# Kernel optimization log

Measured on AMD Instinct MI355X. Metric: run time of the kernel, lower is better.

The kernel has to match this reference:

```python
import jax, jax.numpy as jnp
import numpy as np

EPS = 1e-5

def _layernorm(x, g, b):
    mu = jnp.mean(x, axis=-1, keepdims=True)
    var = jnp.mean(jnp.square(x - mu), axis=-1, keepdims=True)
    return (x - mu) / jnp.sqrt(var + EPS) * g + b

def setup_inputs() -> dict:
    key = jax.random.key(0)
    ks = jax.random.split(key, 8)
    B, T, E, H, Dh, F = 4, 2048, 1024, 16, 64, 4096
    s = lambda fan: 1.0 / np.sqrt(fan)
    return {
        "x":  jax.random.normal(ks[0], (B, T, E), jnp.float32),
        "Wq": jax.random.normal(ks[1], (H, E, Dh), jnp.float32) * s(E),
        "Wk": jax.random.normal(ks[2], (H, E, Dh), jnp.float32) * s(E),
        "Wv": jax.random.normal(ks[3], (H, E, Dh), jnp.float32) * s(E),
        "Wo": jax.random.normal(ks[4], (E, E), jnp.float32) * s(E),
        "bo": jnp.zeros((E,), jnp.float32),
        "W1": jax.random.normal(ks[5], (E, F), jnp.float32) * s(E),
        "b1": jnp.zeros((F,), jnp.float32),
        "W2": jax.random.normal(ks[6], (F, E), jnp.float32) * s(F),
        "b2": jnp.zeros((E,), jnp.float32),
        "g1": jnp.ones((E,), jnp.float32),
        "bt1": jnp.zeros((E,), jnp.float32),
        "g2": jnp.ones((E,), jnp.float32),
        "bt2": jnp.zeros((E,), jnp.float32),
    }

def reference(x, Wq, Wk, Wv, Wo, bo, W1, b1, W2, b2, g1, bt1, g2, bt2):
    B, T, E = x.shape
    # --- pre-LN multi-head attention (dropout = identity in eval) ---
    h = _layernorm(x, g1, bt1)
    q = jnp.einsum('btc,hcd->bhtd', h, Wq)
    k = jnp.einsum('btc,hcd->bhtd', h, Wk)
    v = jnp.einsum('btc,hcd->bhtd', h, Wv)
    # NOTE: original scales by embed_size**-0.5 (input channel c), not head_size
    scores = jnp.einsum('bhtd,bhsd->bhts', q, k) * (E ** -0.5)
    causal = jnp.tril(jnp.ones((T, T), bool))
    scores = jnp.where(causal, scores, -jnp.inf)
    attn = jax.nn.softmax(scores, axis=-1)
    ctx = jnp.einsum('bhts,bhsd->bhtd', attn, v)
    ctx = ctx.transpose(0, 2, 1, 3).reshape(B, T, E)  # concat heads
    x = x + ctx @ Wo + bo
    # --- pre-LN feed-forward ---
    h2 = _layernorm(x, g2, bt2)
    x = x + jax.nn.relu(h2 @ W1 + b1) @ W2 + b2
    return x
```

## Files before the change

kernel.cpp:

```cpp
#include <hip/hip_runtime.h>

typedef unsigned short u16;
typedef __attribute__((ext_vector_type(8))) short bf16x8;
typedef __attribute__((ext_vector_type(4))) short bf16x4;
typedef __attribute__((ext_vector_type(4))) float f32x4;

#define LOG2E 1.4426950408889634f

__device__ __forceinline__ float b2f(u16 u) {
  union { unsigned int i; float f; } x; x.i = ((unsigned int)u) << 16; return x.f;
}
__device__ __forceinline__ u16 f2b(float f) {
  unsigned int i = __float_as_uint(f);
  unsigned int r = (i + 0x7FFFu + ((i >> 16) & 1u)) >> 16;
  return (u16)r;
}
__device__ __forceinline__ void stc(u16* C, size_t i, float v) { C[i] = f2b(v); }
__device__ __forceinline__ void stc(float* C, size_t i, float v) { C[i] = v; }

__device__ __forceinline__ bool is_f32(const unsigned* probe) {
  return probe[0] == 0x3F800000u;
}
__device__ __forceinline__ float ldin(const void* p, size_t i, bool f32) {
  return f32 ? ((const float*)p)[i] : b2f(((const u16*)p)[i]);
}

__device__ __forceinline__ void gld_lds16(const void* g, void* l) {
  __builtin_amdgcn_global_load_lds(
      (const __attribute__((address_space(1))) unsigned int*)g,
      (__attribute__((address_space(3))) unsigned int*)l, 16, 0, 0);
}

__device__ __forceinline__ void lds_wave_fence() {
  __asm__ volatile("s_waitcnt lgkmcnt(0)" ::: "memory");
}

__global__ __launch_bounds__(256) void ln_kernel(
    const void* __restrict__ x, int x_raw,
    const void* __restrict__ g, const void* __restrict__ b,
    u16* __restrict__ y, const unsigned* __restrict__ probe) {
  __shared__ float red[4];
  const bool f32 = is_f32(probe);
  int row = blockIdx.x, tid = threadIdx.x;
  int w = tid >> 6;
  float f0, f1, f2, f3;
  if (x_raw && f32) {
    const float* xr = (const float*)x + (size_t)row * 1024 + tid * 4;
    float4 v = *(const float4*)xr;
    f0 = v.x; f1 = v.y; f2 = v.z; f3 = v.w;
  } else {
    const u16* xr = (const u16*)x + (size_t)row * 1024 + tid * 4;
    bf16x4 v = *(const bf16x4*)xr;
    f0 = b2f((u16)v[0]); f1 = b2f((u16)v[1]); f2 = b2f((u16)v[2]); f3 = b2f((u16)v[3]);
  }
  float s = f0 + f1 + f2 + f3;
  #pragma unroll
  for (int o = 32; o >= 1; o >>= 1) s += __shfl_xor(s, o, 64);
  if ((tid & 63) == 0) red[w] = s;
  __syncthreads();
  float mean = (red[0] + red[1] + red[2] + red[3]) * (1.0f / 1024.0f);
  __syncthreads();
  float d0 = f0 - mean, d1 = f1 - mean, d2 = f2 - mean, d3 = f3 - mean;
  float vs = d0 * d0 + d1 * d1 + d2 * d2 + d3 * d3;
  #pragma unroll
  for (int o = 32; o >= 1; o >>= 1) vs += __shfl_xor(vs, o, 64);
  if ((tid & 63) == 0) red[w] = vs;
  __syncthreads();
  float var = (red[0] + red[1] + red[2] + red[3]) * (1.0f / 1024.0f);
  float rstd = rsqrtf(var + 1e-5f);
  int c = tid * 4;
  float o0 = d0 * rstd * ldin(g, c + 0, f32) + ldin(b, c + 0, f32);
  float o1 = d1 * rstd * ldin(g, c + 1, f32) + ldin(b, c + 1, f32);
  float o2 = d2 * rstd * ldin(g, c + 2, f32) + ldin(b, c + 2, f32);
  float o3 = d3 * rstd * ldin(g, c + 3, f32) + ldin(b, c + 3, f32);
  bf16x4 ov; ov[0] = (short)f2b(o0); ov[1] = (short)f2b(o1);
  ov[2] = (short)f2b(o2); ov[3] = (short)f2b(o3);
  *(bf16x4*)(y + (size_t)row * 1024 + c) = ov;
}

__global__ __launch_bounds__(256) void repack_t(
    const void* __restrict__ src, u16* __restrict__ dst, int N, int K,
    const unsigned* __restrict__ probe) {
  const bool f32 = is_f32(probe);
  int flat = blockIdx.x * 256 + threadIdx.x;
  int n = flat % N;
  int c0 = (flat / N) * 8;
  bf16x8 t;
  #pragma unroll
  for (int j = 0; j < 8; j++) t[j] = (short)f2b(ldin(src, (size_t)(c0 + j) * N + n, f32));
  *(bf16x8*)&dst[(size_t)n * K + c0] = t;
}

__global__ __launch_bounds__(256) void repack_qkv(
    const void* __restrict__ Wq, const void* __restrict__ Wk,
    const void* __restrict__ Wv, u16* __restrict__ dst,
    const unsigned* __restrict__ probe) {
  const bool f32 = is_f32(probe);
  int flat = blockIdx.x * 256 + threadIdx.x;
  int n = flat % 3072;
  int c0 = (flat / 3072) * 8;
  const void* W = (n < 1024) ? Wq : (n < 2048) ? Wk : Wv;
  int nn = n & 1023;
  int hn = nn >> 6, d = nn & 63;
  bf16x8 t;
  #pragma unroll
  for (int j = 0; j < 8; j++)
    t[j] = (short)f2b(ldin(W, (size_t)hn * 65536 + (size_t)(c0 + j) * 64 + d, f32));
  *(bf16x8*)&dst[(size_t)n * 1024 + c0] = t;
}

template <int EPI, typename CT>
__global__ __launch_bounds__(256) void gemm_bt(
    const u16* __restrict__ A, const u16* __restrict__ Bt, CT* __restrict__ C,
    int M, int N, int K, const void* __restrict__ bias,
    const void* __restrict__ res, int res_raw,
    const unsigned* __restrict__ probe) {
  __shared__ __align__(16) u16 sA[128 * 32];
  __shared__ __align__(16) u16 sB[128 * 32];
  const bool f32 = is_f32(probe);
  int tid = threadIdx.x;
  int w = tid >> 6, lane = tid & 63;
  int l15 = lane & 15, q4 = lane >> 4;
  int bm = blockIdx.x * 128, bn = blockIdx.y * 128;
  int wm = (w & 1) * 64, wn = (w >> 1) * 64;
  f32x4 acc[4][4] = {};
  for (int k0 = 0; k0 < K; k0 += 32) {
    #pragma unroll
    for (int j = 0; j < 2; ++j) {
      int c = j * 256 + tid;
      int row = c >> 2, ck = (c & 3) * 8;
      gld_lds16(A + (size_t)(bm + row) * K + k0 + ck, &sA[c * 8]);
    }
    #pragma unroll
    for (int j = 0; j < 2; ++j) {
      int c = j * 256 + tid;
      int row = c >> 2, ck = (c & 3) * 8;
      gld_lds16(Bt + (size_t)(bn + row) * K + k0 + ck, &sB[c * 8]);
    }
    __syncthreads();
    bf16x8 af[4], bf[4];
    #pragma unroll
    for (int i = 0; i < 4; i++) af[i] = *(const bf16x8*)&sA[(wm + i * 16 + l15) * 32 + q4 * 8];
    #pragma unroll
    for (int j = 0; j < 4; j++) bf[j] = *(const bf16x8*)&sB[(wn + j * 16 + l15) * 32 + q4 * 8];
    #pragma unroll
    for (int i = 0; i < 4; i++)
      #pragma unroll
      for (int j = 0; j < 4; j++)
        acc[i][j] = __builtin_amdgcn_mfma_f32_16x16x32_bf16(af[i], bf[j], acc[i][j], 0, 0, 0);
    __syncthreads();
  }
  #pragma unroll
  for (int i = 0; i < 4; i++) {
    int rg = bm + wm + i * 16 + q4 * 4;
    #pragma unroll
    for (int j = 0; j < 4; j++) {
      int cg = bn + wn + j * 16 + l15;
      float bv = (EPI > 0) ? ldin(bias, cg, f32) : 0.0f;
      #pragma unroll
      for (int r = 0; r < 4; r++) {
        float v = acc[i][j][r];
        if (EPI == 1) v += bv + ldin(res, (size_t)(rg + r) * N + cg, res_raw && f32);
        if (EPI == 2) { v += bv; v = fmaxf(v, 0.0f); }
        stc(C, (size_t)(rg + r) * N + cg, v);
      }
    }
  }
}

__global__ __launch_bounds__(256) void attn_kernel(
    const u16* __restrict__ qkv, u16* __restrict__ ctx, int T) {
  __shared__ __align__(16) u16 sK[64 * 64];
  __shared__ __align__(16) u16 sVt[64 * 64];
  __shared__ __align__(16) u16 sP[4 * 16 * 64];
  int tid = threadIdx.x;
  int w = tid >> 6, lane = tid & 63;
  int l15 = lane & 15, q4 = lane >> 4;
  int qtile = blockIdx.x, h = blockIdx.y, b = blockIdx.z;
  int bbase = b * T;
  int qt0 = qtile * 64;

  const u16* qrow = qkv + (size_t)(bbase + qt0 + w * 16 + l15) * 3072 + h * 64;
  bf16x8 qf0 = *(const bf16x8*)(qrow + q4 * 8);
  bf16x8 qf1 = *(const bf16x8*)(qrow + 32 + q4 * 8);

  f32x4 o[4] = {};
  float m4[4] = {-1e30f, -1e30f, -1e30f, -1e30f};
  float l4[4] = {0.f, 0.f, 0.f, 0.f};

  for (int kt = 0; kt <= qtile; ++kt) {
    __syncthreads();
    #pragma unroll
    for (int j = 0; j < 2; ++j) {
      int c = j * 256 + tid;
      int tr = c >> 3, dc = (c & 7) * 8;
      *(bf16x8*)&sK[tr * 64 + dc] =
          *(const bf16x8*)(qkv + (size_t)(bbase + kt * 64 + tr) * 3072 + 1024 + h * 64 + dc);
    }
    {
      int t = tid & 63, dbase = (tid >> 6) * 16;
      const u16* vsrc = qkv + (size_t)(bbase + kt * 64 + t) * 3072 + 2048 + h * 64 + dbase;
      bf16x8 v0 = *(const bf16x8*)vsrc;
      bf16x8 v1 = *(const bf16x8*)(vsrc + 8);
      #pragma unroll
      for (int jj = 0; jj < 8; jj++) {
        sVt[(dbase + jj) * 64 + t] = (u16)v0[jj];
        sVt[(dbase + 8 + jj) * 64 + t] = (u16)v1[jj];
      }
    }
    __syncthreads();

    f32x4 s[4];
    #pragma unroll
    for (int j = 0; j < 4; j++) {
      bf16x8 kf0 = *(const bf16x8*)&sK[(j * 16 + l15) * 64 + q4 * 8];
      bf16x8 kf1 = *(const bf16x8*)&sK[(j * 16 + l15) * 64 + 32 + q4 * 8];
      f32x4 z = {0.f, 0.f, 0.f, 0.f};
      z = __builtin_amdgcn_mfma_f32_16x16x32_bf16(qf0, kf0, z, 0, 0, 0);
      z = __builtin_amdgcn_mfma_f32_16x16x32_bf16(qf1, kf1, z, 0, 0, 0);
      s[j] = z;
    }
    float sv[4][4];
    #pragma unroll
    for (int j = 0; j < 4; j++)
      #pragma unroll
      for (int r = 0; r < 4; r++) {
        float v = s[j][r] * 0.03125f;
        if (kt == qtile && (j * 16 + l15) > (w * 16 + q4 * 4 + r)) v = -1e30f;
        sv[j][r] = v;
      }
    float tm4[4];
    #pragma unroll
    for (int r = 0; r < 4; r++)
      tm4[r] = fmaxf(fmaxf(sv[0][r], sv[1][r]), fmaxf(sv[2][r], sv[3][r]));
    #pragma unroll
    for (int off = 8; off >= 1; off >>= 1)
      #pragma unroll
      for (int r = 0; r < 4; r++) tm4[r] = fmaxf(tm4[r], __shfl_xor(tm4[r], off, 64));
    float al4[4];
    #pragma unroll
    for (int r = 0; r < 4; r++) {
      float mn = fmaxf(m4[r], tm4[r]);
      al4[r] = exp2f((m4[r] - mn) * LOG2E);
      m4[r] = mn;
    }
    float p[4][4], ts4[4];
    #pragma unroll
    for (int j = 0; j < 4; j++)
      #pragma unroll
      for (int r = 0; r < 4; r++) p[j][r] = exp2f((sv[j][r] - m4[r]) * LOG2E);
    #pragma unroll
    for (int r = 0; r < 4; r++) ts4[r] = p[0][r] + p[1][r] + p[2][r] + p[3][r];
    #pragma unroll
    for (int off = 8; off >= 1; off >>= 1)
      #pragma unroll
      for (int r = 0; r < 4; r++) ts4[r] += __shfl_xor(ts4[r], off, 64);
    #pragma unroll
    for (int r = 0; r < 4; r++) l4[r] = l4[r] * al4[r] + ts4[r];
    #pragma unroll
    for (int j = 0; j < 4; j++)
      #pragma unroll
      for (int r = 0; r < 4; r++) o[j][r] *= al4[r];
    #pragma unroll
    for (int j = 0; j < 4; j++)
      #pragma unroll
      for (int r = 0; r < 4; r++)
        sP[w * 1024 + (q4 * 4 + r) * 64 + j * 16 + l15] = f2b(p[j][r]);
    lds_wave_fence();
    bf16x8 pf0 = *(const bf16x8*)&sP[w * 1024 + l15 * 64 + q4 * 8];
    bf16x8 pf1 = *(const bf16x8*)&sP[w * 1024 + l15 * 64 + 32 + q4 * 8];
    #pragma unroll
    for (int j = 0; j < 4; j++) {
      bf16x8 vf0 = *(const bf16x8*)&sVt[(j * 16 + l15) * 64 + q4 * 8];
      bf16x8 vf1 = *(const bf16x8*)&sVt[(j * 16 + l15) * 64 + 32 + q4 * 8];
      o[j] = __builtin_amdgcn_mfma_f32_16x16x32_bf16(pf0, vf0, o[j], 0, 0, 0);
      o[j] = __builtin_amdgcn_mfma_f32_16x16x32_bf16(pf1, vf1, o[j], 0, 0, 0);
    }
  }
  #pragma unroll
  for (int j = 0; j < 4; j++)
    #pragma unroll
    for (int r = 0; r < 4; r++) {
      size_t addr = (size_t)(bbase + qt0 + w * 16 + q4 * 4 + r) * 1024 + h * 64 + j * 16 + l15;
      ctx[addr] = f2b(o[j][r] / l4[r]);
    }
}

extern "C" void kernel_launch(void* const* d_in, const int* in_sizes, int n_in,
                              void* d_out, int out_size, void* d_ws, size_t ws_size,
                              hipStream_t stream) {
  (void)in_sizes; (void)n_in; (void)out_size; (void)ws_size;
  const void* x   = d_in[0];
  const void* Wq  = d_in[1];
  const void* Wk  = d_in[2];
  const void* Wv  = d_in[3];
  const void* Wo  = d_in[4];
  const void* bo  = d_in[5];
  const void* W1  = d_in[6];
  const void* b1  = d_in[7];
  const void* W2  = d_in[8];
  const void* b2  = d_in[9];
  const void* g1  = d_in[10];
  const void* bt1 = d_in[11];
  const void* g2  = d_in[12];
  const void* bt2 = d_in[13];
  const unsigned* probe = (const unsigned*)g1;
  float* out = (float*)d_out;

  const int BT = 8192, T = 2048;
  char* ws = (char*)d_ws;
  u16* hln    = (u16*)(ws);
  u16* qkv    = (u16*)(ws + 16777216);
  u16* ctx    = (u16*)(ws + 16777216 + 50331648);
  u16* a      = (u16*)(ws + 16777216);
  u16* x1     = (u16*)(ws + 83886080);
  u16* wqkv_t = (u16*)(ws + 100663296);
  u16* wo_t   = (u16*)(ws + 106954752);
  u16* w1_t   = (u16*)(ws + 109051904);
  u16* w2_t   = (u16*)(ws + 117440512);

  repack_qkv<<<1536, 256, 0, stream>>>(Wq, Wk, Wv, wqkv_t, probe);
  repack_t<<<512, 256, 0, stream>>>(Wo, wo_t, 1024, 1024, probe);
  repack_t<<<2048, 256, 0, stream>>>(W1, w1_t, 4096, 1024, probe);
  repack_t<<<2048, 256, 0, stream>>>(W2, w2_t, 1024, 4096, probe);

  ln_kernel<<<BT, 256, 0, stream>>>(x, 1, g1, bt1, hln, probe);
  gemm_bt<0, u16><<<dim3(64, 24), 256, 0, stream>>>(hln, wqkv_t, qkv, BT, 3072, 1024,
                                                    nullptr, nullptr, 0, probe);
  attn_kernel<<<dim3(32, 16, 4), 256, 0, stream>>>(qkv, ctx, T);
  gemm_bt<1, u16><<<dim3(64, 8), 256, 0, stream>>>(ctx, wo_t, x1, BT, 1024, 1024,
                                                   bo, x, 1, probe);
  ln_kernel<<<BT, 256, 0, stream>>>(x1, 0, g2, bt2, hln, probe);
  gemm_bt<2, u16><<<dim3(64, 32), 256, 0, stream>>>(hln, w1_t, a, BT, 4096, 1024,
                                                    b1, nullptr, 0, probe);
  gemm_bt<1, float><<<dim3(64, 8), 256, 0, stream>>>(a, w2_t, out, BT, 1024, 4096,
                                                     b2, x1, 0, probe);
}
```

Measured before the change: 827.3 us.

## Restructure attention: 128-row query tiles, padded LDS, shuffle V transpose, balanced scheduling

The attention kernel now processes 128 query rows per block (two 16-row groups per wave), so each K/V tile loaded into LDS is reused by twice as many queries. LDS rows are padded to 68 elements to reduce bank conflicts, and V is transposed in registers via lane shuffles before a vectorized LDS store. Global loads are issued before the barrier to overlap with the previous iteration. The grid is flattened with a causal-balancing tile order. It also skips fully masked sub-tiles and uses the hardware exp2. In exchange, register pressure rises and there are half as many blocks.

```diff
diff --git a/kernel.cpp b/kernel.cpp
--- a/kernel.cpp
+++ b/kernel.cpp
@@ -33,6 +33,21 @@
 
 __device__ __forceinline__ void lds_wave_fence() {
   __asm__ volatile("s_waitcnt lgkmcnt(0)" ::: "memory");
+}
+
+__device__ __forceinline__ void tr8(unsigned a[4], int lane) {
+  unsigned p0, p1, p2, p3;
+  p0 = __shfl_xor((int)a[0], 1, 64); p1 = __shfl_xor((int)a[1], 1, 64);
+  p2 = __shfl_xor((int)a[2], 1, 64); p3 = __shfl_xor((int)a[3], 1, 64);
+  unsigned sel = (lane & 1) ? 0x3276u : 0x5410u;
+  a[0] = __byte_perm(a[0], p0, sel); a[1] = __byte_perm(a[1], p1, sel);
+  a[2] = __byte_perm(a[2], p2, sel); a[3] = __byte_perm(a[3], p3, sel);
+  p0 = __shfl_xor((int)a[0], 2, 64); p1 = __shfl_xor((int)a[1], 2, 64);
+  p2 = __shfl_xor((int)a[2], 2, 64); p3 = __shfl_xor((int)a[3], 2, 64);
+  if (lane & 2) { a[0] = p1; a[2] = p3; } else { a[1] = p0; a[3] = p2; }
+  p0 = __shfl_xor((int)a[0], 4, 64); p1 = __shfl_xor((int)a[1], 4, 64);
+  p2 = __shfl_xor((int)a[2], 4, 64); p3 = __shfl_xor((int)a[3], 4, 64);
+  if (lane & 4) { a[0] = p2; a[1] = p3; } else { a[2] = p0; a[3] = p1; }
 }
 
 __global__ __launch_bounds__(256) void ln_kernel(
@@ -170,120 +185,164 @@
 
 __global__ __launch_bounds__(256) void attn_kernel(
     const u16* __restrict__ qkv, u16* __restrict__ ctx, int T) {
-  __shared__ __align__(16) u16 sK[64 * 64];
-  __shared__ __align__(16) u16 sVt[64 * 64];
-  __shared__ __align__(16) u16 sP[4 * 16 * 64];
+  __shared__ __align__(16) u16 sK[64 * 68];
+  __shared__ __align__(16) u16 sVt[64 * 68];
+  __shared__ __align__(16) u16 sP[8 * 16 * 68];
   int tid = threadIdx.x;
   int w = tid >> 6, lane = tid & 63;
   int l15 = lane & 15, q4 = lane >> 4;
-  int qtile = blockIdx.x, h = blockIdx.y, b = blockIdx.z;
-  int bbase = b * T;
-  int qt0 = qtile * 64;
-
-  const u16* qrow = qkv + (size_t)(bbase + qt0 + w * 16 + l15) * 3072 + h * 64;
-  bf16x8 qf0 = *(const bf16x8*)(qrow + q4 * 8);
-  bf16x8 qf1 = *(const bf16x8*)(qrow + 32 + q4 * 8);
-
-  f32x4 o[4] = {};
-  float m4[4] = {-1e30f, -1e30f, -1e30f, -1e30f};
-  float l4[4] = {0.f, 0.f, 0.f, 0.f};
-
-  for (int kt = 0; kt <= qtile; ++kt) {
-    __syncthreads();
+
+  int n = blockIdx.x;
+  int qi = n & 15;
+  int h = (n >> 4) & 15;
+  int b = (n >> 8) & 3;
+  int qbase = (qi & 1) ? (qi >> 1) : (15 - (qi >> 1));
+  int qt = (qbase + 7 * b) & 15;
+  int qt0 = qt * 128;
+  int mb[2] = {qt0 + w * 16, qt0 + 64 + w * 16};
+  size_t b3072 = (size_t)(b * T) * 3072;
+
+  bf16x8 qf[2][2];
+  #pragma unroll
+  for (int m = 0; m < 2; m++) {
+    const u16* qr = qkv + b3072 + (size_t)(mb[m] + l15) * 3072 + h * 64;
+    qf[m][0] = *(const bf16x8*)(qr + q4 * 8);
+    qf[m][1] = *(const bf16x8*)(qr + 32 + q4 * 8);
+  }
+  f32x4 o[2][4] = {};
+  float mx[2][4], ls[2][4];
+  #pragma unroll
+  for (int m = 0; m < 2; m++)
+    #pragma unroll
+    for (int r = 0; r < 4; r++) { mx[m][r] = -1e30f; ls[m][r] = 0.f; }
+
+  int ktmax = 2 * qt + 1;
+  for (int kt = 0; kt <= ktmax; ++kt) {
+    int s0 = kt * 64;
+    bf16x8 kreg[2]; int krow[2], kcol[2];
     #pragma unroll
     for (int j = 0; j < 2; ++j) {
       int c = j * 256 + tid;
-      int tr = c >> 3, dc = (c & 7) * 8;
-      *(bf16x8*)&sK[tr * 64 + dc] =
-          *(const bf16x8*)(qkv + (size_t)(bbase + kt * 64 + tr) * 3072 + 1024 + h * 64 + dc);
-    }
+      krow[j] = c >> 3; kcol[j] = (c & 7) * 8;
+      kreg[j] = *(const bf16x8*)(qkv + b3072 + (size_t)(s0 + krow[j]) * 3072 + 1024 + h * 64 + kcol[j]);
+    }
+    unsigned va[4], vb[4];
     {
-      int t = tid & 63, dbase = (tid >> 6) * 16;
-      const u16* vsrc = qkv + (size_t)(bbase + kt * 64 + t) * 3072 + 2048 + h * 64 + dbase;
-      bf16x8 v0 = *(const bf16x8*)vsrc;
-      bf16x8 v1 = *(const bf16x8*)(vsrc + 8);
-      #pragma unroll
-      for (int jj = 0; jj < 8; jj++) {
-        sVt[(dbase + jj) * 64 + t] = (u16)v0[jj];
-        sVt[(dbase + 8 + jj) * 64 + t] = (u16)v1[jj];
-      }
+      const u16* vs = qkv + b3072 + (size_t)(s0 + lane) * 3072 + 2048 + h * 64 + w * 16;
+      *(bf16x8*)va = *(const bf16x8*)vs;
+      *(bf16x8*)vb = *(const bf16x8*)(vs + 8);
     }
     __syncthreads();
-
-    f32x4 s[4];
-    #pragma unroll
-    for (int j = 0; j < 4; j++) {
-      bf16x8 kf0 = *(const bf16x8*)&sK[(j * 16 + l15) * 64 + q4 * 8];
-      bf16x8 kf1 = *(const bf16x8*)&sK[(j * 16 + l15) * 64 + 32 + q4 * 8];
+    #pragma unroll
+    for (int j = 0; j < 2; ++j)
+      *(bf16x8*)&sK[krow[j] * 68 + kcol[j]] = kreg[j];
+    tr8(va, lane); tr8(vb, lane);
+    {
+      int dd = w * 16 + (lane & 7), t0 = (lane >> 3) * 8;
+      *(bf16x8*)&sVt[dd * 68 + t0] = *(bf16x8*)va;
+      *(bf16x8*)&sVt[(dd + 8) * 68 + t0] = *(bf16x8*)vb;
+    }
+    __syncthreads();
+
+    bool act0 = (s0 <= mb[0] + 15);
+    f32x4 s[2][4];
+    #pragma unroll
+    for (int j = 0; j < 4; ++j) {
+      bf16x8 k0 = *(const bf16x8*)&sK[(j * 16 + l15) * 68 + q4 * 8];
+      bf16x8 k1 = *(const bf16x8*)&sK[(j * 16 + l15) * 68 + 32 + q4 * 8];
+      if (act0) {
+        f32x4 z = {0.f, 0.f, 0.f, 0.f};
+        z = __builtin_amdgcn_mfma_f32_16x16x32_bf16(qf[0][0], k0, z, 0, 0, 0);
+        s[0][j] = __builtin_amdgcn_mfma_f32_16x16x32_bf16(qf[0][1], k1, z, 0, 0, 0);
+      }
       f32x4 z = {0.f, 0.f, 0.f, 0.f};
-      z = __builtin_amdgcn_mfma_f32_16x16x32_bf16(qf0, kf0, z, 0, 0, 0);
-      z = __builtin_amdgcn_mfma_f32_16x16x32_bf16(qf1, kf1, z, 0, 0, 0);
-      s[j] = z;
-    }
-    float sv[4][4];
-    #pragma unroll
-    for (int j = 0; j < 4; j++)
-      #pragma unroll
-      for (int r = 0; r < 4; r++) {
-        float v = s[j][r] * 0.03125f;
-        if (kt == qtile && (j * 16 + l15) > (w * 16 + q4 * 4 + r)) v = -1e30f;
-        sv[j][r] = v;
-      }
-    float tm4[4];
-    #pragma unroll
-    for (int r = 0; r < 4; r++)
-      tm4[r] = fmaxf(fmaxf(sv[0][r], sv[1][r]), fmaxf(sv[2][r], sv[3][r]));
-    #pragma unroll
-    for (int off = 8; off >= 1; off >>= 1)
-      #pragma unroll
-      for (int r = 0; r < 4; r++) tm4[r] = fmaxf(tm4[r], __shfl_xor(tm4[r], off, 64));
-    float al4[4];
-    #pragma unroll
-    for (int r = 0; r < 4; r++) {
-      float mn = fmaxf(m4[r], tm4[r]);
-      al4[r] = exp2f((m4[r] - mn) * LOG2E);
-      m4[r] = mn;
-    }
-    float p[4][4], ts4[4];
-    #pragma unroll
-    for (int j = 0; j < 4; j++)
-      #pragma unroll
-      for (int r = 0; r < 4; r++) p[j][r] = exp2f((sv[j][r] - m4[r]) * LOG2E);
-    #pragma unroll
-    for (int r = 0; r < 4; r++) ts4[r] = p[0][r] + p[1][r] + p[2][r] + p[3][r];
-    #pragma unroll
-    for (int off = 8; off >= 1; off >>= 1)
-      #pragma unroll
-      for (int r = 0; r < 4; r++) ts4[r] += __shfl_xor(ts4[r], off, 64);
-    #pragma unroll
-    for (int r = 0; r < 4; r++) l4[r] = l4[r] * al4[r] + ts4[r];
-    #pragma unroll
-    for (int j = 0; j < 4; j++)
-      #pragma unroll
-      for (int r = 0; r < 4; r++) o[j][r] *= al4[r];
-    #pragma unroll
-    for (int j = 0; j < 4; j++)
-      #pragma unroll
-      for (int r = 0; r < 4; r++)
-        sP[w * 1024 + (q4 * 4 + r) * 64 + j * 16 + l15] = f2b(p[j][r]);
+      z = __builtin_amdgcn_mfma_f32_16x16x32_bf16(qf[1][0], k0, z, 0, 0, 0);
+      s[1][j] = __builtin_amdgcn_mfma_f32_16x16x32_bf16(qf[1][1], k1, z, 0, 0, 0);
+    }
+    #pragma unroll
+    for (int m = 0; m < 2; ++m) {
+      if (m == 0 && !act0) continue;
+      int mbm = mb[m];
+      if (s0 + 63 > mbm) {
+        #pragma unroll
+        for (int j = 0; j < 4; ++j)
+          #pragma unroll
+          for (int r = 0; r < 4; ++r) {
+            float v = s[m][j][r] * 0.03125f;
+            if (s0 + j * 16 + l15 > mbm + q4 * 4 + r) v = -1e30f;
+            s[m][j][r] = v;
+          }
+      } else {
+        #pragma unroll
+        for (int j = 0; j < 4; ++j)
+          #pragma unroll
+          for (int r = 0; r < 4; ++r) s[m][j][r] *= 0.03125f;
+      }
+      float tm[4];
+      #pragma unroll
+      for (int r = 0; r < 4; ++r)
+        tm[r] = fmaxf(fmaxf(s[m][0][r], s[m][1][r]), fmaxf(s[m][2][r], s[m][3][r]));
+      #pragma unroll
+      for (int off = 8; off >= 1; off >>= 1)
+        #pragma unroll
+        for (int r = 0; r < 4; ++r) tm[r] = fmaxf(tm[r], __shfl_xor(tm[r], off, 64));
+      float al[4], ts[4];
+      #pragma unroll
+      for (int r = 0; r < 4; ++r) {
+        float mn = fmaxf(mx[m][r], tm[r]);
+        al[r] = __builtin_amdgcn_exp2f((mx[m][r] - mn) * LOG2E);
+        mx[m][r] = mn; ts[r] = 0.f;
+      }
+      int pbase = (w * 2 + m) * 1088;
+      #pragma unroll
+      for (int j = 0; j < 4; ++j)
+        #pragma unroll
+        for (int r = 0; r < 4; ++r) {
+          float p = __builtin_amdgcn_exp2f((s[m][j][r] - mx[m][r]) * LOG2E);
+          ts[r] += p;
+          sP[pbase + (q4 * 4 + r) * 68 + j * 16 + l15] = f2b(p);
+        }
+      #pragma unroll
+      for (int off = 8; off >= 1; off >>= 1)
+        #pragma unroll
+        for (int r = 0; r < 4; ++r) ts[r] += __shfl_xor(ts[r], off, 64);
+      #pragma unroll
+      for (int r = 0; r < 4; ++r) ls[m][r] = ls[m][r] * al[r] + ts[r];
+      #pragma unroll
+      for (int j = 0; j < 4; ++j)
+        #pragma unroll
+        for (int r = 0; r < 4; ++r) o[m][j][r] *= al[r];
+    }
     lds_wave_fence();
-    bf16x8 pf0 = *(const bf16x8*)&sP[w * 1024 + l15 * 64 + q4 * 8];
-    bf16x8 pf1 = *(const bf16x8*)&sP[w * 1024 + l15 * 64 + 32 + q4 * 8];
-    #pragma unroll
-    for (int j = 0; j < 4; j++) {
-      bf16x8 vf0 = *(const bf16x8*)&sVt[(j * 16 + l15) * 64 + q4 * 8];
-      bf16x8 vf1 = *(const bf16x8*)&sVt[(j * 16 + l15) * 64 + 32 + q4 * 8];
-      o[j] = __builtin_amdgcn_mfma_f32_16x16x32_bf16(pf0, vf0, o[j], 0, 0, 0);
-      o[j] = __builtin_amdgcn_mfma_f32_16x16x32_bf16(pf1, vf1, o[j], 0, 0, 0);
-    }
-  }
-  #pragma unroll
-  for (int j = 0; j < 4; j++)
-    #pragma unroll
-    for (int r = 0; r < 4; r++) {
-      size_t addr = (size_t)(bbase + qt0 + w * 16 + q4 * 4 + r) * 1024 + h * 64 + j * 16 + l15;
-      ctx[addr] = f2b(o[j][r] / l4[r]);
-    }
+    bf16x8 pf[2][2];
+    #pragma unroll
+    for (int m = 0; m < 2; ++m) {
+      if (m == 0 && !act0) continue;
+      int pbase = (w * 2 + m) * 1088;
+      pf[m][0] = *(const bf16x8*)&sP[pbase + l15 * 68 + q4 * 8];
+      pf[m][1] = *(const bf16x8*)&sP[pbase + l15 * 68 + 32 + q4 * 8];
+    }
+    #pragma unroll
+    for (int j = 0; j < 4; ++j) {
+      bf16x8 vf0 = *(const bf16x8*)&sVt[(j * 16 + l15) * 68 + q4 * 8];
+      bf16x8 vf1 = *(const bf16x8*)&sVt[(j * 16 + l15) * 68 + 32 + q4 * 8];
+      if (act0) {
+        o[0][j] = __builtin_amdgcn_mfma_f32_16x16x32_bf16(pf[0][0], vf0, o[0][j], 0, 0, 0);
+        o[0][j] = __builtin_amdgcn_mfma_f32_16x16x32_bf16(pf[0][1], vf1, o[0][j], 0, 0, 0);
+      }
+      o[1][j] = __builtin_amdgcn_mfma_f32_16x16x32_bf16(pf[1][0], vf0, o[1][j], 0, 0, 0);
+      o[1][j] = __builtin_amdgcn_mfma_f32_16x16x32_bf16(pf[1][1], vf1, o[1][j], 0, 0, 0);
+    }
+  }
+  #pragma unroll
+  for (int m = 0; m < 2; ++m)
+    #pragma unroll
+    for (int j = 0; j < 4; ++j)
+      #pragma unroll
+      for (int r = 0; r < 4; ++r) {
+        size_t addr = (size_t)(b * T + mb[m] + q4 * 4 + r) * 1024 + h * 64 + j * 16 + l15;
+        ctx[addr] = f2b(o[m][j][r] / ls[m][r]);
+      }
 }
 
 extern "C" void kernel_launch(void* const* d_in, const int* in_sizes, int n_in,
@@ -327,7 +386,7 @@
   ln_kernel<<<BT, 256, 0, stream>>>(x, 1, g1, bt1, hln, probe);
   gemm_bt<0, u16><<<dim3(64, 24), 256, 0, stream>>>(hln, wqkv_t, qkv, BT, 3072, 1024,
                                                     nullptr, nullptr, 0, probe);
-  attn_kernel<<<dim3(32, 16, 4), 256, 0, stream>>>(qkv, ctx, T);
+  attn_kernel<<<1024, 256, 0, stream>>>(qkv, ctx, T);
   gemm_bt<1, u16><<<dim3(64, 8), 256, 0, stream>>>(ctx, wo_t, x1, BT, 1024, 1024,
                                                    bo, x, 1, probe);
   ln_kernel<<<BT, 256, 0, stream>>>(x1, 0, g2, bt2, hln, probe);
```

New measurement: 803.2 us. 1.03x faster.
